# Kernel tuning notes

Hardware: AMD Instinct MI355X
Metric: run time of the kernel (lower is better)

## Reference

```python
import jax, jax.numpy as jnp
import numpy as np

N, E, H = 50000, 800000, 128
EPS = 1e-5

def _init(key, shape, fan_in):
    return jax.random.normal(key, shape, dtype=jnp.float32) / np.sqrt(fan_in)

def setup_inputs() -> dict:
    key = jax.random.key(0)
    ks = jax.random.split(key, 20)
    x = jax.random.normal(ks[0], (N, 3), dtype=jnp.float32)
    h = jax.random.normal(ks[1], (N, H), dtype=jnp.float32)
    edge_index = jax.random.randint(ks[2], (2, E), 0, N, dtype=jnp.int32)
    d_ei = 2 * H + 1
    return {
        "x": x, "h": h, "edge_index": edge_index,
        "We1": _init(ks[3], (d_ei, H), d_ei), "be1": jnp.zeros((H,), jnp.float32),
        "We2": _init(ks[4], (H, H), H),       "be2": jnp.zeros((H,), jnp.float32),
        "Wc1": _init(ks[5], (H, H), H),       "bc1": jnp.zeros((H,), jnp.float32),
        "Wc2": _init(ks[6], (H, 1), H),       "bc2": jnp.zeros((1,), jnp.float32),
        "Wn1": _init(ks[7], (2 * H, H), 2 * H), "bn1": jnp.zeros((H,), jnp.float32),
        "Wn2": _init(ks[8], (H, H), H),       "bn2": jnp.zeros((H,), jnp.float32),
        "gamma": jnp.ones((H,), jnp.float32), "beta": jnp.zeros((H,), jnp.float32),
    }

def reference(x, h, edge_index, We1, be1, We2, be2, Wc1, bc1, Wc2, bc2,
              Wn1, bn1, Wn2, bn2, gamma, beta):
    act = jax.nn.silu
    row, col = edge_index[0], edge_index[1]
    n = x.shape[0]
    rel = x[row] - x[col]                                  # [E,3]
    dist2 = jnp.sum(rel * rel, axis=-1, keepdims=True)     # [E,1]
    edge_input = jnp.concatenate([h[row], h[col], dist2], axis=-1)  # [E,2H+1]
    ef = act(edge_input @ We1 + be1)
    ef = act(ef @ We2 + be2)                                # [E,H]
    gate = act(ef @ Wc1 + bc1) @ Wc2 + bc2                  # [E,1]
    # scatter-mean by row (shared counts for coords and features)
    counts = jax.ops.segment_sum(jnp.ones((rel.shape[0], 1), x.dtype), row, num_segments=n)
    counts = jnp.clip(counts, 1.0)
    dx = jax.ops.segment_sum(rel * gate, row, num_segments=n) / counts
    x_out = x + dx
    agg = jax.ops.segment_sum(ef, row, num_segments=n) / counts     # [N,H]
    dh = act(jnp.concatenate([h, agg], axis=-1) @ Wn1 + bn1) @ Wn2 + bn2
    h2 = h + dh
    mu = jnp.mean(h2, axis=-1, keepdims=True)
    var = jnp.mean((h2 - mu) ** 2, axis=-1, keepdims=True)
    h_norm = (h2 - mu) / jnp.sqrt(var + EPS) * gamma + beta
    h_out = act(h_norm)
    return x_out, h_out
```

## Files before the change

kernel.cpp:

```cpp
#include <hip/hip_runtime.h>

#define NN 50000
#define NE 800000
#define HD 128

typedef __attribute__((ext_vector_type(4))) float vf32x4;
typedef __attribute__((ext_vector_type(8))) __bf16 vbf16x8;
typedef __attribute__((ext_vector_type(4))) unsigned short vushort4;
typedef __attribute__((ext_vector_type(8))) unsigned short vushort8;

constexpr size_t OFF_AGG  = 0;
constexpr size_t OFF_CNT  = 25600000;
constexpr size_t OFF_DX   = 25800000;
constexpr size_t ZBYTES   = 26400000;
constexpr size_t OFF_HBF  = 26400000;
constexpr size_t OFF_WE1P = 39200000;
constexpr size_t OFF_WE2P = OFF_WE1P + 65536;
constexpr size_t OFF_WC1P = OFF_WE2P + 32768;
constexpr size_t OFF_WN1P = OFF_WC1P + 32768;
constexpr size_t OFF_WN2P = OFF_WN1P + 65536;

__device__ __forceinline__ unsigned short f2bf(float f) {
    unsigned int u = __float_as_uint(f);
    u += 0x7fffu + ((u >> 16) & 1u);
    return (unsigned short)(u >> 16);
}

__device__ __forceinline__ float silu(float v) {
    return __fdividef(v, 1.0f + __expf(-v));
}

__global__ __launch_bounds__(256) void h2bf_kernel(const float* __restrict__ h,
                                                   unsigned short* __restrict__ h_bf) {
    int idx = blockIdx.x * 256 + threadIdx.x;
    vf32x4 v = ((const vf32x4*)h)[idx];
    vushort4 o;
    o[0] = f2bf(v[0]); o[1] = f2bf(v[1]); o[2] = f2bf(v[2]); o[3] = f2bf(v[3]);
    ((vushort4*)h_bf)[idx] = o;
}

__device__ __forceinline__ void pack_one(const float* __restrict__ src,
                                         unsigned short* __restrict__ dst,
                                         int local, int KB) {
    int j = local & 7;
    int lane = (local >> 3) & 63;
    int rest = local >> 9;
    int kb = rest % KB;
    int t = rest / KB;
    int srow = kb * 32 + ((lane >> 4) << 3) + j;
    int scol = t * 16 + (lane & 15);
    dst[local] = f2bf(src[srow * 128 + scol]);
}

__global__ __launch_bounds__(256) void pack_w_kernel(
    const float* __restrict__ We1, const float* __restrict__ We2,
    const float* __restrict__ Wc1, const float* __restrict__ Wn1,
    const float* __restrict__ Wn2,
    unsigned short* __restrict__ We1p, unsigned short* __restrict__ We2p,
    unsigned short* __restrict__ Wc1p, unsigned short* __restrict__ Wn1p,
    unsigned short* __restrict__ Wn2p) {
    int idx = blockIdx.x * 256 + threadIdx.x;
    if (idx < 32768)       pack_one(We1, We1p, idx, 8);
    else if (idx < 49152)  pack_one(We2, We2p, idx - 32768, 4);
    else if (idx < 65536)  pack_one(Wc1, Wc1p, idx - 49152, 4);
    else if (idx < 98304)  pack_one(Wn1, Wn1p, idx - 65536, 8);
    else                   pack_one(Wn2, Wn2p, idx - 98304, 4);
}

__global__ __launch_bounds__(256, 4) void edge_kernel(
    const float* __restrict__ x, const int* __restrict__ ei,
    const unsigned short* __restrict__ h_bf,
    const unsigned short* __restrict__ We1p, const unsigned short* __restrict__ We2p,
    const unsigned short* __restrict__ Wc1p,
    const float* __restrict__ We1, const float* __restrict__ be1,
    const float* __restrict__ be2, const float* __restrict__ bc1,
    const float* __restrict__ Wc2, const float* __restrict__ bc2,
    float* __restrict__ counts, float* __restrict__ dxsum, float* __restrict__ agg) {

    __shared__ __align__(16) unsigned short s_ef[64 * 136];
    __shared__ float s_rel[64 * 4];
    __shared__ int s_row[64];
    __shared__ int s_col[64];

    const int tid = threadIdx.x;
    const int ebase = blockIdx.x * 64;

    if (tid < 64) {
        int e = ebase + tid;
        int r = ei[e], c = ei[NE + e];
        s_row[tid] = r;
        s_col[tid] = c;
        float d0 = x[r * 3 + 0] - x[c * 3 + 0];
        float d1 = x[r * 3 + 1] - x[c * 3 + 1];
        float d2v = x[r * 3 + 2] - x[c * 3 + 2];
        s_rel[tid * 4 + 0] = d0;
        s_rel[tid * 4 + 1] = d1;
        s_rel[tid * 4 + 2] = d2v;
        s_rel[tid * 4 + 3] = d0 * d0 + d1 * d1 + d2v * d2v;
    }
    __syncthreads();

    const int wave = tid >> 6, lane = tid & 63;
    const int li = lane & 15, grp = lane >> 4;
    const int el = wave * 16 + li;
    const vf32x4 vzero = {0.f, 0.f, 0.f, 0.f};

    vbf16x8 af[8];
    {
        const unsigned short* pr = h_bf + (size_t)s_row[el] * 128 + grp * 8;
        const unsigned short* pc = h_bf + (size_t)s_col[el] * 128 + grp * 8;
#pragma unroll
        for (int kb = 0; kb < 4; kb++) af[kb] = *(const vbf16x8*)(pr + kb * 32);
#pragma unroll
        for (int kb = 0; kb < 4; kb++) af[4 + kb] = *(const vbf16x8*)(pc + kb * 32);
    }

    vf32x4 acc[8];
#pragma unroll
    for (int t = 0; t < 8; t++) acc[t] = vzero;
#pragma unroll
    for (int kb = 0; kb < 8; kb++) {
#pragma unroll
        for (int t = 0; t < 8; t++) {
            vbf16x8 b = *(const vbf16x8*)(We1p + ((t * 8 + kb) * 64 + lane) * 8);
            acc[t] = __builtin_amdgcn_mfma_f32_16x16x32_bf16(af[kb], b, acc[t], 0, 0, 0);
        }
    }
    float d2[4];
#pragma unroll
    for (int r = 0; r < 4; r++) d2[r] = s_rel[(wave * 16 + grp * 4 + r) * 4 + 3];
#pragma unroll
    for (int t = 0; t < 8; t++) {
        int col = t * 16 + li;
        float b1 = be1[col], wl = We1[256 * 128 + col];
#pragma unroll
        for (int r = 0; r < 4; r++) {
            float v = silu(acc[t][r] + b1 + d2[r] * wl);
            s_ef[(wave * 16 + grp * 4 + r) * 136 + col] = f2bf(v);
        }
    }
    __syncthreads();

#pragma unroll
    for (int t = 0; t < 8; t++) acc[t] = vzero;
    {
        const unsigned short* arow = s_ef + (wave * 16 + li) * 136 + grp * 8;
#pragma unroll
        for (int kb = 0; kb < 4; kb++) {
            vbf16x8 a = *(const vbf16x8*)(arow + kb * 32);
#pragma unroll
            for (int t = 0; t < 8; t++) {
                vbf16x8 b = *(const vbf16x8*)(We2p + ((t * 4 + kb) * 64 + lane) * 8);
                acc[t] = __builtin_amdgcn_mfma_f32_16x16x32_bf16(a, b, acc[t], 0, 0, 0);
            }
        }
    }
    float ef_reg[8][4];
#pragma unroll
    for (int t = 0; t < 8; t++) {
        float b2 = be2[t * 16 + li];
#pragma unroll
        for (int r = 0; r < 4; r++) ef_reg[t][r] = silu(acc[t][r] + b2);
    }
    __syncthreads();
#pragma unroll
    for (int t = 0; t < 8; t++) {
        int col = t * 16 + li;
#pragma unroll
        for (int r = 0; r < 4; r++)
            s_ef[(wave * 16 + grp * 4 + r) * 136 + col] = f2bf(ef_reg[t][r]);
    }
    __syncthreads();

#pragma unroll
    for (int t = 0; t < 8; t++) acc[t] = vzero;
    {
        const unsigned short* arow = s_ef + (wave * 16 + li) * 136 + grp * 8;
#pragma unroll
        for (int kb = 0; kb < 4; kb++) {
            vbf16x8 a = *(const vbf16x8*)(arow + kb * 32);
#pragma unroll
            for (int t = 0; t < 8; t++) {
                vbf16x8 b = *(const vbf16x8*)(Wc1p + ((t * 4 + kb) * 64 + lane) * 8);
                acc[t] = __builtin_amdgcn_mfma_f32_16x16x32_bf16(a, b, acc[t], 0, 0, 0);
            }
        }
    }
    float gp[4] = {0.f, 0.f, 0.f, 0.f};
#pragma unroll
    for (int t = 0; t < 8; t++) {
        int col = t * 16 + li;
        float bc = bc1[col], w2 = Wc2[col];
#pragma unroll
        for (int r = 0; r < 4; r++) gp[r] += silu(acc[t][r] + bc) * w2;
    }
#pragma unroll
    for (int r = 0; r < 4; r++) {
#pragma unroll
        for (int d = 1; d < 16; d <<= 1) gp[r] += __shfl_xor(gp[r], d, 16);
        gp[r] += bc2[0];
    }

#pragma unroll
    for (int r = 0; r < 4; r++) {
        int e2 = wave * 16 + grp * 4 + r;
        int node = s_row[e2];
#pragma unroll
        for (int t = 0; t < 8; t++)
            atomicAdd(&agg[(size_t)node * 128 + t * 16 + li], ef_reg[t][r]);
        if (li < 3)
            atomicAdd(&dxsum[node * 3 + li], s_rel[e2 * 4 + li] * gp[r]);
        else if (li == 3)
            atomicAdd(&counts[node], 1.0f);
    }
}

__global__ __launch_bounds__(256, 4) void node_kernel(
    const float* __restrict__ x, const float* __restrict__ h32,
    const unsigned short* __restrict__ h_bf,
    const float* __restrict__ counts, const float* __restrict__ dxsum,
    const float* __restrict__ agg,
    const unsigned short* __restrict__ Wn1p, const unsigned short* __restrict__ Wn2p,
    const float* __restrict__ bn1, const float* __restrict__ bn2,
    const float* __restrict__ gamma, const float* __restrict__ beta,
    float* __restrict__ out) {

    __shared__ __align__(16) unsigned short s_agg[64 * 136];
    __shared__ __align__(16) unsigned short s_ef[64 * 136];

    const int tid = threadIdx.x;
    const int nbase = blockIdx.x * 64;

    {
        int idx = blockIdx.x * 192 + tid;
        if (tid < 192 && idx < NN * 3) {
            int node = idx / 3;
            float cnt = fmaxf(counts[node], 1.0f);
            out[idx] = x[idx] + dxsum[idx] / cnt;
        }
    }
#pragma unroll
    for (int i = 0; i < 8; i++) {
        int flat = i * 256 + tid;
        int row = flat >> 5, q = flat & 31;
        int node = nbase + row;
        if (node >= NN) node = NN - 1;
        float inv = 1.0f / fmaxf(counts[node], 1.0f);
        vf32x4 v = *(const vf32x4*)(agg + (size_t)node * 128 + q * 4);
        vushort4 o;
        o[0] = f2bf(v[0] * inv); o[1] = f2bf(v[1] * inv);
        o[2] = f2bf(v[2] * inv); o[3] = f2bf(v[3] * inv);
        *(vushort4*)(&s_agg[row * 136 + q * 4]) = o;
    }
    __syncthreads();

    const int wave = tid >> 6, lane = tid & 63;
    const int li = lane & 15, grp = lane >> 4;
    const vf32x4 vzero = {0.f, 0.f, 0.f, 0.f};

    int mynode = nbase + wave * 16 + li;
    if (mynode >= NN) mynode = NN - 1;

    vbf16x8 af[8];
    {
        const unsigned short* ph = h_bf + (size_t)mynode * 128 + grp * 8;
#pragma unroll
        for (int kb = 0; kb < 4; kb++) af[kb] = *(const vbf16x8*)(ph + kb * 32);
        const unsigned short* pa = s_agg + (wave * 16 + li) * 136 + grp * 8;
#pragma unroll
        for (int kb = 0; kb < 4; kb++) af[4 + kb] = *(const vbf16x8*)(pa + kb * 32);
    }
    vf32x4 acc[8];
#pragma unroll
    for (int t = 0; t < 8; t++) acc[t] = vzero;
#pragma unroll
    for (int kb = 0; kb < 8; kb++) {
#pragma unroll
        for (int t = 0; t < 8; t++) {
            vbf16x8 b = *(const vbf16x8*)(Wn1p + ((t * 8 + kb) * 64 + lane) * 8);
            acc[t] = __builtin_amdgcn_mfma_f32_16x16x32_bf16(af[kb], b, acc[t], 0, 0, 0);
        }
    }
#pragma unroll
    for (int t = 0; t < 8; t++) {
        int col = t * 16 + li;
        float b1 = bn1[col];
#pragma unroll
        for (int r = 0; r < 4; r++) {
            float v = silu(acc[t][r] + b1);
            s_ef[(wave * 16 + grp * 4 + r) * 136 + col] = f2bf(v);
        }
    }
    __syncthreads();

#pragma unroll
    for (int t = 0; t < 8; t++) acc[t] = vzero;
    {
        const unsigned short* arow = s_ef + (wave * 16 + li) * 136 + grp * 8;
#pragma unroll
        for (int kb = 0; kb < 4; kb++) {
            vbf16x8 a = *(const vbf16x8*)(arow + kb * 32);
#pragma unroll
            for (int t = 0; t < 8; t++) {
                vbf16x8 b = *(const vbf16x8*)(Wn2p + ((t * 4 + kb) * 64 + lane) * 8);
                acc[t] = __builtin_amdgcn_mfma_f32_16x16x32_bf16(a, b, acc[t], 0, 0, 0);
            }
        }
    }
    float h2v[8][4];
    float sum[4] = {0.f, 0.f, 0.f, 0.f}, sq[4] = {0.f, 0.f, 0.f, 0.f};
#pragma unroll
    for (int t = 0; t < 8; t++) {
        int col = t * 16 + li;
        float b2 = bn2[col];
#pragma unroll
        for (int r = 0; r < 4; r++) {
            int node = nbase + wave * 16 + grp * 4 + r;
            int nc = node < NN ? node : NN - 1;
            float v = acc[t][r] + b2 + h32[(size_t)nc * 128 + col];
            h2v[t][r] = v;
            sum[r] += v;
            sq[r] += v * v;
        }
    }
    float mu[4], rstd[4];
#pragma unroll
    for (int r = 0; r < 4; r++) {
#pragma unroll
        for (int d = 1; d < 16; d <<= 1) {
            sum[r] += __shfl_xor(sum[r], d, 16);
            sq[r] += __shfl_xor(sq[r], d, 16);
        }
        mu[r] = sum[r] * (1.0f / 128.0f);
        float var = sq[r] * (1.0f / 128.0f) - mu[r] * mu[r];
        rstd[r] = rsqrtf(var + 1e-5f);
    }
#pragma unroll
    for (int t = 0; t < 8; t++) {
        int col = t * 16 + li;
        float g = gamma[col], bt = beta[col];
#pragma unroll
        for (int r = 0; r < 4; r++) {
            int node = nbase + wave * 16 + grp * 4 + r;
            if (node < NN) {
                float vn = (h2v[t][r] - mu[r]) * rstd[r] * g + bt;
                out[NN * 3 + (size_t)node * 128 + col] = silu(vn);
            }
        }
    }
}

extern "C" void kernel_launch(void* const* d_in, const int* in_sizes, int n_in,
                              void* d_out, int out_size, void* d_ws, size_t ws_size,
                              hipStream_t stream) {
    const float* x     = (const float*)d_in[0];
    const float* h     = (const float*)d_in[1];
    const int* ei      = (const int*)d_in[2];
    const float* We1   = (const float*)d_in[3];
    const float* be1   = (const float*)d_in[4];
    const float* We2   = (const float*)d_in[5];
    const float* be2   = (const float*)d_in[6];
    const float* Wc1   = (const float*)d_in[7];
    const float* bc1   = (const float*)d_in[8];
    const float* Wc2   = (const float*)d_in[9];
    const float* bc2   = (const float*)d_in[10];
    const float* Wn1   = (const float*)d_in[11];
    const float* bn1   = (const float*)d_in[12];
    const float* Wn2   = (const float*)d_in[13];
    const float* bn2   = (const float*)d_in[14];
    const float* gamma = (const float*)d_in[15];
    const float* beta  = (const float*)d_in[16];
    float* out = (float*)d_out;

    char* ws = (char*)d_ws;
    float* agg            = (float*)(ws + OFF_AGG);
    float* counts         = (float*)(ws + OFF_CNT);
    float* dxsum          = (float*)(ws + OFF_DX);
    unsigned short* h_bf  = (unsigned short*)(ws + OFF_HBF);
    unsigned short* We1p  = (unsigned short*)(ws + OFF_WE1P);
    unsigned short* We2p  = (unsigned short*)(ws + OFF_WE2P);
    unsigned short* Wc1p  = (unsigned short*)(ws + OFF_WC1P);
    unsigned short* Wn1p  = (unsigned short*)(ws + OFF_WN1P);
    unsigned short* Wn2p  = (unsigned short*)(ws + OFF_WN2P);

    hipMemsetAsync(ws, 0, ZBYTES, stream);
    h2bf_kernel<<<NN * 128 / 4 / 256, 256, 0, stream>>>(h, h_bf);
    pack_w_kernel<<<114688 / 256, 256, 0, stream>>>(We1, We2, Wc1, Wn1, Wn2,
                                                    We1p, We2p, Wc1p, Wn1p, Wn2p);
    edge_kernel<<<NE / 64, 256, 0, stream>>>(x, ei, h_bf, We1p, We2p, Wc1p,
                                             We1, be1, be2, bc1, Wc2, bc2,
                                             counts, dxsum, agg);
    node_kernel<<<(NN + 63) / 64, 256, 0, stream>>>(x, h, h_bf, counts, dxsum, agg,
                                                    Wn1p, Wn2p, bn1, bn2, gamma, beta, out);
}
```

Measured before the change: 618.0 us.

## Sort edges by row via counting sort and pre-combine same-row atomics

Adds histogram, single-block scan and scatter kernels that bucket the edges by destination row into a packed (row,col) array. The edge kernel reads this sorted list and merges consecutive edges with the same row in registers before issuing atomicAdds to agg and dxsum. Counts now come from the integer histogram instead of float atomics. The aim is to cut global atomic traffic and contention and to improve locality of the scatter. In exchange it adds three extra launches, including a serial one-block scan over 50k nodes, and its own atomic-based scatter pass.

After: 685.5 us. +10.9%, slower.

```diff
diff --git a/kernel.cpp b/kernel.cpp
--- a/kernel.cpp
+++ b/kernel.cpp
@@ -2,7 +2,6 @@
 
 #define NN 50000
 #define NE 800000
-#define HD 128
 
 typedef __attribute__((ext_vector_type(4))) float vf32x4;
 typedef __attribute__((ext_vector_type(8))) __bf16 vbf16x8;
@@ -13,8 +12,10 @@
 constexpr size_t OFF_CNT  = 25600000;
 constexpr size_t OFF_DX   = 25800000;
 constexpr size_t ZBYTES   = 26400000;
-constexpr size_t OFF_HBF  = 26400000;
-constexpr size_t OFF_WE1P = 39200000;
+constexpr size_t OFF_OFFS = 26400000;
+constexpr size_t OFF_RC2  = 26600000;
+constexpr size_t OFF_HBF  = 33000000;
+constexpr size_t OFF_WE1P = 45800000;
 constexpr size_t OFF_WE2P = OFF_WE1P + 65536;
 constexpr size_t OFF_WC1P = OFF_WE2P + 32768;
 constexpr size_t OFF_WN1P = OFF_WC1P + 32768;
@@ -67,15 +68,69 @@
     else                   pack_one(Wn2, Wn2p, idx - 98304, 4);
 }
 
+__global__ __launch_bounds__(256) void hist_kernel(const int* __restrict__ ei,
+                                                   int* __restrict__ cnt) {
+    int e = blockIdx.x * 256 + threadIdx.x;
+    if (e < NE) atomicAdd(&cnt[ei[e]], 1);
+}
+
+__global__ __launch_bounds__(1024) void scan_kernel(const int* __restrict__ cnt,
+                                                    int* __restrict__ offs) {
+    __shared__ int wsum[16];
+    __shared__ int wpre[16];
+    __shared__ int carry;
+    int tid = threadIdx.x, lane = tid & 63, w = tid >> 6;
+    if (tid == 0) carry = 0;
+    __syncthreads();
+    for (int base = 0; base < NN; base += 1024) {
+        int idx = base + tid;
+        int v = (idx < NN) ? cnt[idx] : 0;
+        int s = v;
+#pragma unroll
+        for (int d = 1; d < 64; d <<= 1) {
+            int t2 = __shfl_up(s, d, 64);
+            if (lane >= d) s += t2;
+        }
+        if (lane == 63) wsum[w] = s;
+        __syncthreads();
+        if (w == 0 && lane < 16) {
+            int ws2 = wsum[lane];
+#pragma unroll
+            for (int d = 1; d < 16; d <<= 1) {
+                int t2 = __shfl_up(ws2, d, 16);
+                if (lane >= d) ws2 += t2;
+            }
+            wpre[lane] = ws2;
+        }
+        __syncthreads();
+        int excl = (w ? wpre[w - 1] : 0) + carry + (s - v);
+        if (idx < NN) offs[idx] = excl;
+        __syncthreads();
+        if (tid == 1023) carry += wpre[15];
+        __syncthreads();
+    }
+}
+
+__global__ __launch_bounds__(256) void scatter_kernel(const int* __restrict__ ei,
+                                                      int* __restrict__ offs,
+                                                      int2* __restrict__ rc2) {
+    int e = blockIdx.x * 256 + threadIdx.x;
+    if (e < NE) {
+        int r = ei[e], c = ei[NE + e];
+        int p = atomicAdd(&offs[r], 1);
+        rc2[p] = make_int2(r, c);
+    }
+}
+
 __global__ __launch_bounds__(256, 4) void edge_kernel(
-    const float* __restrict__ x, const int* __restrict__ ei,
+    const float* __restrict__ x, const int2* __restrict__ rc2,
     const unsigned short* __restrict__ h_bf,
     const unsigned short* __restrict__ We1p, const unsigned short* __restrict__ We2p,
     const unsigned short* __restrict__ Wc1p,
     const float* __restrict__ We1, const float* __restrict__ be1,
     const float* __restrict__ be2, const float* __restrict__ bc1,
     const float* __restrict__ Wc2, const float* __restrict__ bc2,
-    float* __restrict__ counts, float* __restrict__ dxsum, float* __restrict__ agg) {
+    float* __restrict__ dxsum, float* __restrict__ agg) {
 
     __shared__ __align__(16) unsigned short s_ef[64 * 136];
     __shared__ float s_rel[64 * 4];
@@ -86,8 +141,8 @@
     const int ebase = blockIdx.x * 64;
 
     if (tid < 64) {
-        int e = ebase + tid;
-        int r = ei[e], c = ei[NE + e];
+        int2 rc = rc2[ebase + tid];
+        int r = rc.x, c = rc.y;
         s_row[tid] = r;
         s_col[tid] = c;
         float d0 = x[r * 3 + 0] - x[c * 3 + 0];
@@ -201,24 +256,44 @@
         gp[r] += bc2[0];
     }
 
-#pragma unroll
-    for (int r = 0; r < 4; r++) {
-        int e2 = wave * 16 + grp * 4 + r;
-        int node = s_row[e2];
+    {
+        const int q0 = wave * 16 + grp * 4;
+        int cur = s_row[q0];
+        float av[8];
+#pragma unroll
+        for (int t = 0; t < 8; t++) av[t] = ef_reg[t][0];
+        float dxa = (li < 3) ? s_rel[q0 * 4 + li] * gp[0] : 0.f;
+#pragma unroll
+        for (int r = 1; r < 4; r++) {
+            int rw = s_row[q0 + r];
+            if (rw != cur) {
+#pragma unroll
+                for (int t = 0; t < 8; t++) {
+                    atomicAdd(&agg[(size_t)cur * 128 + t * 16 + li], av[t]);
+                    av[t] = ef_reg[t][r];
+                }
+                if (li < 3) {
+                    atomicAdd(&dxsum[cur * 3 + li], dxa);
+                    dxa = s_rel[(q0 + r) * 4 + li] * gp[r];
+                }
+                cur = rw;
+            } else {
+#pragma unroll
+                for (int t = 0; t < 8; t++) av[t] += ef_reg[t][r];
+                if (li < 3) dxa += s_rel[(q0 + r) * 4 + li] * gp[r];
+            }
+        }
 #pragma unroll
         for (int t = 0; t < 8; t++)
-            atomicAdd(&agg[(size_t)node * 128 + t * 16 + li], ef_reg[t][r]);
-        if (li < 3)
-            atomicAdd(&dxsum[node * 3 + li], s_rel[e2 * 4 + li] * gp[r]);
-        else if (li == 3)
-            atomicAdd(&counts[node], 1.0f);
+            atomicAdd(&agg[(size_t)cur * 128 + t * 16 + li], av[t]);
+        if (li < 3) atomicAdd(&dxsum[cur * 3 + li], dxa);
     }
 }
 
 __global__ __launch_bounds__(256, 4) void node_kernel(
     const float* __restrict__ x, const float* __restrict__ h32,
     const unsigned short* __restrict__ h_bf,
-    const float* __restrict__ counts, const float* __restrict__ dxsum,
+    const int* __restrict__ cnt, const float* __restrict__ dxsum,
     const float* __restrict__ agg,
     const unsigned short* __restrict__ Wn1p, const unsigned short* __restrict__ Wn2p,
     const float* __restrict__ bn1, const float* __restrict__ bn2,
@@ -235,8 +310,8 @@
         int idx = blockIdx.x * 192 + tid;
         if (tid < 192 && idx < NN * 3) {
             int node = idx / 3;
-            float cnt = fmaxf(counts[node], 1.0f);
-            out[idx] = x[idx] + dxsum[idx] / cnt;
+            float cf = fmaxf((float)cnt[node], 1.0f);
+            out[idx] = x[idx] + dxsum[idx] / cf;
         }
     }
 #pragma unroll
@@ -245,7 +320,7 @@
         int row = flat >> 5, q = flat & 31;
         int node = nbase + row;
         if (node >= NN) node = NN - 1;
-        float inv = 1.0f / fmaxf(counts[node], 1.0f);
+        float inv = 1.0f / fmaxf((float)cnt[node], 1.0f);
         vf32x4 v = *(const vf32x4*)(agg + (size_t)node * 128 + q * 4);
         vushort4 o;
         o[0] = f2bf(v[0] * inv); o[1] = f2bf(v[1] * inv);
@@ -374,8 +449,10 @@
 
     char* ws = (char*)d_ws;
     float* agg            = (float*)(ws + OFF_AGG);
-    float* counts         = (float*)(ws + OFF_CNT);
+    int* cnt              = (int*)(ws + OFF_CNT);
     float* dxsum          = (float*)(ws + OFF_DX);
+    int* offs             = (int*)(ws + OFF_OFFS);
+    int2* rc2             = (int2*)(ws + OFF_RC2);
     unsigned short* h_bf  = (unsigned short*)(ws + OFF_HBF);
     unsigned short* We1p  = (unsigned short*)(ws + OFF_WE1P);
     unsigned short* We2p  = (unsigned short*)(ws + OFF_WE2P);
@@ -384,12 +461,15 @@
     unsigned short* Wn2p  = (unsigned short*)(ws + OFF_WN2P);
 
     hipMemsetAsync(ws, 0, ZBYTES, stream);
-    h2bf_kernel<<<NN * 128 / 4 / 256, 256, 0, stream>>>(h, h_bf);
-    pack_w_kernel<<<114688 / 256, 256, 0, stream>>>(We1, We2, Wc1, Wn1, Wn2,
-                                                    We1p, We2p, Wc1p, Wn1p, Wn2p);
-    edge_kernel<<<NE / 64, 256, 0, stream>>>(x, ei, h_bf, We1p, We2p, Wc1p,
+    h2bf_kernel<<<6250, 256, 0, stream>>>(h, h_bf);
+    pack_w_kernel<<<448, 256, 0, stream>>>(We1, We2, Wc1, Wn1, Wn2,
+                                           We1p, We2p, Wc1p, Wn1p, Wn2p);
+    hist_kernel<<<NE / 256, 256, 0, stream>>>(ei, cnt);
+    scan_kernel<<<1, 1024, 0, stream>>>(cnt, offs);
+    scatter_kernel<<<NE / 256, 256, 0, stream>>>(ei, offs, rc2);
+    edge_kernel<<<NE / 64, 256, 0, stream>>>(x, rc2, h_bf, We1p, We2p, Wc1p,
                                              We1, be1, be2, bc1, Wc2, bc2,
-                                             counts, dxsum, agg);
-    node_kernel<<<(NN + 63) / 64, 256, 0, stream>>>(x, h, h_bf, counts, dxsum, agg,
+                                             dxsum, agg);
+    node_kernel<<<(NN + 63) / 64, 256, 0, stream>>>(x, h, h_bf, cnt, dxsum, agg,
                                                     Wn1p, Wn2p, bn1, bn2, gamma, beta, out);
 }
```

## Make edge and node kernels wave-local, drop block barriers, split degree histogram

Applied to the files above, without the earlier changes.

Restructures edge_kernel and node_kernel so each wave loads its own 16 edges or nodes and owns its own rows of shared memory, which lets every __syncthreads be removed. Edge degree counting moves out of the edge kernel into a separate integer-atomic histogram kernel. The edge kernel's occupancy hint rises from 4 to 5 blocks per SM, and f2bf now uses the native bf16 conversion. The extra launch and the pass over row indices add work, and the tighter occupancy hint may cause register spills.

After: 677.1 us. 9.6% more time.

```diff
diff --git a/kernel.cpp b/kernel.cpp
--- a/kernel.cpp
+++ b/kernel.cpp
@@ -2,7 +2,6 @@
 
 #define NN 50000
 #define NE 800000
-#define HD 128
 
 typedef __attribute__((ext_vector_type(4))) float vf32x4;
 typedef __attribute__((ext_vector_type(8))) __bf16 vbf16x8;
@@ -21,9 +20,9 @@
 constexpr size_t OFF_WN2P = OFF_WN1P + 65536;
 
 __device__ __forceinline__ unsigned short f2bf(float f) {
-    unsigned int u = __float_as_uint(f);
-    u += 0x7fffu + ((u >> 16) & 1u);
-    return (unsigned short)(u >> 16);
+    union { __bf16 h; unsigned short u; } c;
+    c.h = (__bf16)f;
+    return c.u;
 }
 
 __device__ __forceinline__ float silu(float v) {
@@ -67,7 +66,13 @@
     else                   pack_one(Wn2, Wn2p, idx - 98304, 4);
 }
 
-__global__ __launch_bounds__(256, 4) void edge_kernel(
+__global__ __launch_bounds__(256) void hist_kernel(const int* __restrict__ ei,
+                                                   int* __restrict__ cnt) {
+    int e = blockIdx.x * 256 + threadIdx.x;
+    if (e < NE) atomicAdd(&cnt[ei[e]], 1);
+}
+
+__global__ __launch_bounds__(256, 5) void edge_kernel(
     const float* __restrict__ x, const int* __restrict__ ei,
     const unsigned short* __restrict__ h_bf,
     const unsigned short* __restrict__ We1p, const unsigned short* __restrict__ We2p,
@@ -75,7 +80,7 @@
     const float* __restrict__ We1, const float* __restrict__ be1,
     const float* __restrict__ be2, const float* __restrict__ bc1,
     const float* __restrict__ Wc2, const float* __restrict__ bc2,
-    float* __restrict__ counts, float* __restrict__ dxsum, float* __restrict__ agg) {
+    float* __restrict__ dxsum, float* __restrict__ agg) {
 
     __shared__ __align__(16) unsigned short s_ef[64 * 136];
     __shared__ float s_rel[64 * 4];
@@ -83,26 +88,25 @@
     __shared__ int s_col[64];
 
     const int tid = threadIdx.x;
+    const int wave = tid >> 6, lane = tid & 63;
+    const int li = lane & 15, grp = lane >> 4;
     const int ebase = blockIdx.x * 64;
-
-    if (tid < 64) {
-        int e = ebase + tid;
+    const int el = wave * 16 + li;
+
+    if (lane < 16) {
+        int e = ebase + wave * 16 + lane;
         int r = ei[e], c = ei[NE + e];
-        s_row[tid] = r;
-        s_col[tid] = c;
+        s_row[wave * 16 + lane] = r;
+        s_col[wave * 16 + lane] = c;
         float d0 = x[r * 3 + 0] - x[c * 3 + 0];
         float d1 = x[r * 3 + 1] - x[c * 3 + 1];
         float d2v = x[r * 3 + 2] - x[c * 3 + 2];
-        s_rel[tid * 4 + 0] = d0;
-        s_rel[tid * 4 + 1] = d1;
-        s_rel[tid * 4 + 2] = d2v;
-        s_rel[tid * 4 + 3] = d0 * d0 + d1 * d1 + d2v * d2v;
-    }
-    __syncthreads();
-
-    const int wave = tid >> 6, lane = tid & 63;
-    const int li = lane & 15, grp = lane >> 4;
-    const int el = wave * 16 + li;
+        s_rel[(wave * 16 + lane) * 4 + 0] = d0;
+        s_rel[(wave * 16 + lane) * 4 + 1] = d1;
+        s_rel[(wave * 16 + lane) * 4 + 2] = d2v;
+        s_rel[(wave * 16 + lane) * 4 + 3] = d0 * d0 + d1 * d1 + d2v * d2v;
+    }
+
     const vf32x4 vzero = {0.f, 0.f, 0.f, 0.f};
 
     vbf16x8 af[8];
@@ -139,7 +143,6 @@
             s_ef[(wave * 16 + grp * 4 + r) * 136 + col] = f2bf(v);
         }
     }
-    __syncthreads();
 
 #pragma unroll
     for (int t = 0; t < 8; t++) acc[t] = vzero;
@@ -158,19 +161,14 @@
     float ef_reg[8][4];
 #pragma unroll
     for (int t = 0; t < 8; t++) {
-        float b2 = be2[t * 16 + li];
-#pragma unroll
-        for (int r = 0; r < 4; r++) ef_reg[t][r] = silu(acc[t][r] + b2);
-    }
-    __syncthreads();
-#pragma unroll
-    for (int t = 0; t < 8; t++) {
-        int col = t * 16 + li;
-#pragma unroll
-        for (int r = 0; r < 4; r++)
+        int col = t * 16 + li;
+        float b2 = be2[col];
+#pragma unroll
+        for (int r = 0; r < 4; r++) {
+            ef_reg[t][r] = silu(acc[t][r] + b2);
             s_ef[(wave * 16 + grp * 4 + r) * 136 + col] = f2bf(ef_reg[t][r]);
-    }
-    __syncthreads();
+        }
+    }
 
 #pragma unroll
     for (int t = 0; t < 8; t++) acc[t] = vzero;
@@ -210,15 +208,13 @@
             atomicAdd(&agg[(size_t)node * 128 + t * 16 + li], ef_reg[t][r]);
         if (li < 3)
             atomicAdd(&dxsum[node * 3 + li], s_rel[e2 * 4 + li] * gp[r]);
-        else if (li == 3)
-            atomicAdd(&counts[node], 1.0f);
     }
 }
 
 __global__ __launch_bounds__(256, 4) void node_kernel(
     const float* __restrict__ x, const float* __restrict__ h32,
     const unsigned short* __restrict__ h_bf,
-    const float* __restrict__ counts, const float* __restrict__ dxsum,
+    const int* __restrict__ cnt, const float* __restrict__ dxsum,
     const float* __restrict__ agg,
     const unsigned short* __restrict__ Wn1p, const unsigned short* __restrict__ Wn2p,
     const float* __restrict__ bn1, const float* __restrict__ bn2,
@@ -230,34 +226,32 @@
 
     const int tid = threadIdx.x;
     const int nbase = blockIdx.x * 64;
+    const int wave = tid >> 6, lane = tid & 63;
+    const int li = lane & 15, grp = lane >> 4;
 
     {
         int idx = blockIdx.x * 192 + tid;
         if (tid < 192 && idx < NN * 3) {
             int node = idx / 3;
-            float cnt = fmaxf(counts[node], 1.0f);
-            out[idx] = x[idx] + dxsum[idx] / cnt;
-        }
-    }
-#pragma unroll
-    for (int i = 0; i < 8; i++) {
-        int flat = i * 256 + tid;
-        int row = flat >> 5, q = flat & 31;
-        int node = nbase + row;
+            float cf = fmaxf((float)cnt[node], 1.0f);
+            out[idx] = x[idx] + dxsum[idx] / cf;
+        }
+    }
+#pragma unroll
+    for (int it = 0; it < 8; it++) {
+        int idx = it * 64 + lane;
+        int rloc = idx >> 5, q = idx & 31;
+        int node = nbase + wave * 16 + rloc;
         if (node >= NN) node = NN - 1;
-        float inv = 1.0f / fmaxf(counts[node], 1.0f);
+        float inv = 1.0f / fmaxf((float)cnt[node], 1.0f);
         vf32x4 v = *(const vf32x4*)(agg + (size_t)node * 128 + q * 4);
         vushort4 o;
         o[0] = f2bf(v[0] * inv); o[1] = f2bf(v[1] * inv);
         o[2] = f2bf(v[2] * inv); o[3] = f2bf(v[3] * inv);
-        *(vushort4*)(&s_agg[row * 136 + q * 4]) = o;
-    }
-    __syncthreads();
-
-    const int wave = tid >> 6, lane = tid & 63;
-    const int li = lane & 15, grp = lane >> 4;
+        *(vushort4*)(&s_agg[(wave * 16 + rloc) * 136 + q * 4]) = o;
+    }
+
     const vf32x4 vzero = {0.f, 0.f, 0.f, 0.f};
-
     int mynode = nbase + wave * 16 + li;
     if (mynode >= NN) mynode = NN - 1;
 
@@ -291,7 +285,6 @@
             s_ef[(wave * 16 + grp * 4 + r) * 136 + col] = f2bf(v);
         }
     }
-    __syncthreads();
 
 #pragma unroll
     for (int t = 0; t < 8; t++) acc[t] = vzero;
@@ -374,7 +367,7 @@
 
     char* ws = (char*)d_ws;
     float* agg            = (float*)(ws + OFF_AGG);
-    float* counts         = (float*)(ws + OFF_CNT);
+    int* cnt              = (int*)(ws + OFF_CNT);
     float* dxsum          = (float*)(ws + OFF_DX);
     unsigned short* h_bf  = (unsigned short*)(ws + OFF_HBF);
     unsigned short* We1p  = (unsigned short*)(ws + OFF_WE1P);
@@ -384,12 +377,13 @@
     unsigned short* Wn2p  = (unsigned short*)(ws + OFF_WN2P);
 
     hipMemsetAsync(ws, 0, ZBYTES, stream);
-    h2bf_kernel<<<NN * 128 / 4 / 256, 256, 0, stream>>>(h, h_bf);
-    pack_w_kernel<<<114688 / 256, 256, 0, stream>>>(We1, We2, Wc1, Wn1, Wn2,
-                                                    We1p, We2p, Wc1p, Wn1p, Wn2p);
+    h2bf_kernel<<<6250, 256, 0, stream>>>(h, h_bf);
+    pack_w_kernel<<<448, 256, 0, stream>>>(We1, We2, Wc1, Wn1, Wn2,
+                                           We1p, We2p, Wc1p, Wn1p, Wn2p);
+    hist_kernel<<<NE / 256, 256, 0, stream>>>(ei, cnt);
     edge_kernel<<<NE / 64, 256, 0, stream>>>(x, ei, h_bf, We1p, We2p, Wc1p,
                                              We1, be1, be2, bc1, Wc2, bc2,
-                                             counts, dxsum, agg);
-    node_kernel<<<(NN + 63) / 64, 256, 0, stream>>>(x, h, h_bf, counts, dxsum, agg,
+                                             dxsum, agg);
+    node_kernel<<<(NN + 63) / 64, 256, 0, stream>>>(x, h, h_bf, cnt, dxsum, agg,
                                                     Wn1p, Wn2p, bn1, bn2, gamma, beta, out);
 }
```
